# Performance work log

Measured on AMD Instinct MI355X. Metric: run time of the kernel, lower is better.

Reference implementation:

```python
import jax, jax.numpy as jnp
import numpy as np

LEAK = 0.95
THRESHOLD = 1.0
RESCALE = 2.0


def _xavier_uniform(key, shape, gain=2.0):
    fan_out, fan_in = shape
    bound = gain * np.sqrt(6.0 / (fan_in + fan_out))
    return jax.random.uniform(key, shape, jnp.float32, -bound, bound)


def setup_inputs() -> dict:
    key = jax.random.key(0)
    k_inp, k_w1, k_w2 = jax.random.split(key, 3)
    inp = jax.random.normal(k_inp, (8192, 784), jnp.float32)
    w1 = _xavier_uniform(k_w1, (800, 784))   # fc1.weight
    w2 = _xavier_uniform(k_w2, (10, 800))    # fc2.weight
    return {"inp": inp, "w1": w1, "w2": w2, "num_steps": 25}


@jax.custom_vjp
def spike_fn(x):
    return (x > 0).astype(x.dtype)

def _spike_fwd(x):
    return spike_fn(x), x

def _spike_bwd(x, g):
    # grad = g * 0.3 * relu(1 - |x|)  (surrogate BP)
    return (g * 0.3 * jnp.maximum(1.0 - jnp.abs(x), 0.0),)

spike_fn.defvjp(_spike_fwd, _spike_bwd)


def poisson_gen(key, inp):
    r = jax.random.uniform(key, inp.shape, inp.dtype)
    temp = (r * RESCALE <= jnp.abs(inp)).astype(inp.dtype) * jnp.sign(inp)
    return 0.5 * (temp + 1.0)


def reference(inp, w1, w2, num_steps):
    batch = inp.shape[0]
    x = inp.reshape(batch, -1)
    keys = jax.random.split(jax.random.key(42), num_steps)

    def step(carry, key):
        mem1, mem2 = carry
        sp = poisson_gen(key, x)                    # [B, 784]
        mem1 = LEAK * mem1 + (1.0 - LEAK) * (sp @ w1.T)  # [B, 800]
        mem_thr = mem1 / THRESHOLD - 1.0
        out = spike_fn(mem_thr)
        rst = jnp.where(mem_thr > 0, THRESHOLD, 0.0)
        mem1 = mem1 - jax.lax.stop_gradient(rst)
        mem2 = mem2 + out @ w2.T                    # [B, 10]
        return (mem1, mem2), None

    init = (jnp.zeros((batch, 800), x.dtype), jnp.zeros((batch, 10), x.dtype))
    (_, mem2), _ = jax.lax.scan(step, init, keys)
    return mem2 / num_steps
```

## Files before the change

### kernel.cpp

```cpp
#include <hip/hip_runtime.h>
#include <cstdint>

__host__ __device__ inline uint32_t tf_rotl32(uint32_t x, uint32_t r) {
  return (x << r) | (x >> (32u - r));
}

__host__ __device__ inline void threefry2x32(uint32_t k0, uint32_t k1,
                                             uint32_t x0, uint32_t x1,
                                             uint32_t* o0, uint32_t* o1) {
  uint32_t ks0 = k0, ks1 = k1, ks2 = k0 ^ k1 ^ 0x1BD11BDAu;
  x0 += ks0; x1 += ks1;
#define TF_R(r) { x0 += x1; x1 = tf_rotl32(x1, r); x1 ^= x0; }
  TF_R(13) TF_R(15) TF_R(26) TF_R(6)
  x0 += ks1; x1 += ks2 + 1u;
  TF_R(17) TF_R(29) TF_R(16) TF_R(24)
  x0 += ks2; x1 += ks0 + 2u;
  TF_R(13) TF_R(15) TF_R(26) TF_R(6)
  x0 += ks0; x1 += ks1 + 3u;
  TF_R(17) TF_R(29) TF_R(16) TF_R(24)
  x0 += ks1; x1 += ks2 + 4u;
  TF_R(13) TF_R(15) TF_R(26) TF_R(6)
  x0 += ks2; x1 += ks0 + 5u;
#undef TF_R
  *o0 = x0; *o1 = x1;
}

#define BSZ   8192
#define KIN   784
#define HID   800
#define NOUT  10
#define NSTEP 25


__global__ __launch_bounds__(256) void enc_kernel(const float* __restrict__ inp,
                                                  uint8_t* __restrict__ enc,
                                                  uint32_t k0, uint32_t k1) {
  int j = blockIdx.x * blockDim.x + threadIdx.x;
  if (j >= BSZ * KIN) return;
  uint32_t o0, o1;
  threefry2x32(k0, k1, 0u, (uint32_t)j, &o0, &o1);
  uint32_t bits = o0 ^ o1;
  float r = __uint_as_float((bits >> 9) | 0x3f800000u) - 1.0f;
  float x = inp[j];
  bool cond = (2.0f * r <= fabsf(x));
  int s = (x > 0.0f) ? 1 : ((x < 0.0f) ? -1 : 0);
  enc[j] = (uint8_t)(1 + (cond ? s : 0));
}

#define BM 128
#define BN 32
#define BK 8

typedef float f32x2 __attribute__((ext_vector_type(2)));
typedef uint32_t u32;

__device__ __forceinline__ float cvt_ub(u32 x, int i) {
  return (float)((x >> (8 * i)) & 0xffu);
}

__device__ __forceinline__ void gload4(const void* g, void* l) {
  __builtin_amdgcn_global_load_lds(
      (const __attribute__((address_space(1))) void*)g,
      (__attribute__((address_space(3))) void*)l, 4, 0, 0);
}

__device__ __forceinline__ void pk_fma_lo(f32x2& acc, f32x2 a, f32x2 b) {
  asm("v_pk_fma_f32 %0, %1, %2, %0 op_sel:[0,0,0] op_sel_hi:[0,1,1]"
      : "+v"(acc)
      : "v"(a), "v"(b));
}
__device__ __forceinline__ void pk_fma_hi(f32x2& acc, f32x2 a, f32x2 b) {
  asm("v_pk_fma_f32 %0, %1, %2, %0 op_sel:[1,0,0] op_sel_hi:[1,1,1]"
      : "+v"(acc)
      : "v"(a), "v"(b));
}

__global__ __launch_bounds__(256) void gemm_kernel(const uint8_t* __restrict__ enc,
                                                   const float* __restrict__ w1,
                                                   float* __restrict__ gp) {
  __shared__ u32   As[2][BK * BM / 4];
  __shared__ float Bs[2][BK][BN];
  const int panel  = blockIdx.z;
  const int kstart = panel * 264;
  const int ntile  = (panel == 2) ? 32 : 33;
  const int m0 = blockIdx.x * BM;
  const int n0 = blockIdx.y * BN;
  const int t  = threadIdx.x;
  const int lane = t & 63;
  const int wv   = t >> 6;

  const int tm = t / 8;
  const int tn = t % 8;

  const uint8_t* a_src = enc + (size_t)(m0 + (lane >> 1)) * KIN + kstart + (lane & 1) * 4;
  const float*   b_src = w1  + (size_t)(n0 + (lane & 31)) * KIN + kstart + (lane >> 5);

  f32x2 acc[4][2];
#pragma unroll
  for (int mi = 0; mi < 4; mi++)
#pragma unroll
    for (int nj = 0; nj < 2; nj++) acc[mi][nj] = (f32x2)(0.0f);

#define ISSUE(P, TILE)                                                    \
  {                                                                       \
    if (wv == 0) {                                                        \
      _Pragma("unroll")                                                   \
      for (int q = 0; q < 4; q++)                                         \
        gload4(a_src + (size_t)(TILE) * BK + (size_t)(32 * q) * KIN,      \
               &As[P][64 * q]);                                           \
    } else if (wv == 1) {                                                 \
      _Pragma("unroll")                                                   \
      for (int q = 0; q < 4; q++)                                         \
        gload4(b_src + (size_t)(TILE) * BK + 2 * q, &Bs[P][2 * q][0]);    \
    }                                                                     \
  }

  ISSUE(0, 0)
  __syncthreads();

  int p = 0;
  for (int tile = 0; tile < ntile; tile++) {
    if (tile + 1 < ntile) { ISSUE(p ^ 1, tile + 1) }
    const u32* aw = &As[p][tm * 8];
    uint4 qa = *(const uint4*)(aw);
    uint4 qb = *(const uint4*)(aw + 4);
#pragma unroll
    for (int kk = 0; kk < BK; kk++) {
      const u32 w0  = (kk < 4) ? qa.x : qa.y;
      const u32 w1r = (kk < 4) ? qa.z : qa.w;
      const u32 w2  = (kk < 4) ? qb.x : qb.y;
      const u32 w3  = (kk < 4) ? qb.z : qb.w;
      const int sh = kk & 3;
      f32x2 am[2];
      am[0].x = cvt_ub(w0, sh);  am[0].y = cvt_ub(w1r, sh);
      am[1].x = cvt_ub(w2, sh);  am[1].y = cvt_ub(w3, sh);
      float4 bv = *(const float4*)&Bs[p][kk][tn * 4];
      f32x2 b2[2];
      b2[0].x = bv.x; b2[0].y = bv.y;
      b2[1].x = bv.z; b2[1].y = bv.w;
#pragma unroll
      for (int mp = 0; mp < 2; mp++) {
        pk_fma_lo(acc[2 * mp + 0][0], am[mp], b2[0]);
        pk_fma_lo(acc[2 * mp + 0][1], am[mp], b2[1]);
        pk_fma_hi(acc[2 * mp + 1][0], am[mp], b2[0]);
        pk_fma_hi(acc[2 * mp + 1][1], am[mp], b2[1]);
      }
    }
    __syncthreads();
    p ^= 1;
  }
#undef ISSUE

  float* base = gp + (size_t)panel * BSZ * HID;
#pragma unroll
  for (int mi = 0; mi < 4; mi++) {
    float* dst = base + (size_t)(m0 + tm * 4 + mi) * HID + n0 + tn * 4;
    float4 o;
    o.x = acc[mi][0].x;
    o.y = acc[mi][0].y;
    o.z = acc[mi][1].x;
    o.w = acc[mi][1].y;
    *(float4*)dst = o;
  }
}

__global__ __launch_bounds__(256) void update_kernel(const float* __restrict__ gp,
                                                     float* __restrict__ mem1,
                                                     const float* __restrict__ w2,
                                                     float* __restrict__ mem2) {
  __shared__ float w2s[NOUT * HID];
  for (int i = threadIdx.x; i < NOUT * HID; i += 256) w2s[i] = w2[i];
  __syncthreads();

  const int wave = threadIdx.x / 64;
  const int lane = threadIdx.x % 64;
  const int b = blockIdx.x * 4 + wave;

  const size_t GS = (size_t)BSZ * HID;
  const float* g0 = gp + (size_t)b * HID;
  const float* g1 = g0 + GS;
  const float* g2 = g1 + GS;
  float* mrow = mem1 + (size_t)b * HID;

  float acc[NOUT];
#pragma unroll
  for (int i = 0; i < NOUT; i++) acc[i] = 0.0f;

  for (int j = lane; j < HID; j += 64) {
    float gs = __fmul_rn(0.5f, __fadd_rn(__fadd_rn(g0[j], g1[j]), g2[j]));
    float m = __fadd_rn(__fmul_rn(0.95f, mrow[j]), __fmul_rn(0.05f, gs));
    bool spike = __fadd_rn(m, -1.0f) > 0.0f;
    mrow[j] = spike ? __fadd_rn(m, -1.0f) : m;
    if (spike) {
#pragma unroll
      for (int i = 0; i < NOUT; i++) acc[i] += w2s[i * HID + j];
    }
  }
#pragma unroll
  for (int i = 0; i < NOUT; i++) {
    float v = acc[i];
    for (int off = 32; off > 0; off >>= 1) v += __shfl_down(v, off);
    if (lane == 0) mem2[(size_t)b * NOUT + i] += v;
  }
}

__global__ __launch_bounds__(256) void finalize_kernel(const float* __restrict__ mem2,
                                                       const int* __restrict__ ns,
                                                       float* __restrict__ out) {
  int i = blockIdx.x * blockDim.x + threadIdx.x;
  if (i < BSZ * NOUT) out[i] = mem2[i] / (float)(*ns);
}

extern "C" void kernel_launch(void* const* d_in, const int* in_sizes, int n_in,
                              void* d_out, int out_size, void* d_ws, size_t ws_size,
                              hipStream_t stream) {
  const float* inp = (const float*)d_in[0];
  const float* w1  = (const float*)d_in[1];
  const float* w2  = (const float*)d_in[2];
  const int*   dns = (const int*)d_in[3];
  float* out = (float*)d_out;

  char* ws = (char*)d_ws;
  size_t off = 0;
  uint8_t* enc = (uint8_t*)(ws + off);  off += (size_t)BSZ * KIN;
  off = (off + 255) & ~(size_t)255;
  float* gp   = (float*)(ws + off);     off += (size_t)3 * BSZ * HID * 4;
  float* mem1 = (float*)(ws + off);     off += (size_t)BSZ * HID * 4;
  float* mem2 = (float*)(ws + off);     off += (size_t)BSZ * NOUT * 4;

  (void)hipMemsetAsync(mem1, 0, (size_t)BSZ * HID * 4, stream);
  (void)hipMemsetAsync(mem2, 0, (size_t)BSZ * NOUT * 4, stream);

  uint32_t keys[NSTEP][2];
  for (int t = 0; t < NSTEP; t++)
    threefry2x32(0u, 42u, 0u, (uint32_t)t, &keys[t][0], &keys[t][1]);

  const int n_elem = BSZ * KIN;
  for (int t = 0; t < NSTEP; t++) {
    enc_kernel<<<(n_elem + 255) / 256, 256, 0, stream>>>(inp, enc, keys[t][0], keys[t][1]);
    gemm_kernel<<<dim3(BSZ / BM, HID / BN, 3), 256, 0, stream>>>(enc, w1, gp);
    update_kernel<<<BSZ / 4, 256, 0, stream>>>(gp, mem1, w2, mem2);
  }
  finalize_kernel<<<(BSZ * NOUT + 255) / 256, 256, 0, stream>>>(mem2, dns, out);
}
```

Baseline: 4.857 ms.

## Halve GEMM block threads, give each thread 8x4 outputs with padded A tile

The GEMM block drops from 256 to 128 threads, and each thread now computes 8 rows by 4 columns instead of 4 by 4, which doubles register-level reuse of the B fragment. The A shared tile is regrouped with padding (AGRP=68) so each thread reads its 8-row fragment with four 16-byte LDS loads while avoiding bank conflicts. Wave 0 still loads A and wave 1 loads B. Fewer threads per block and more accumulator registers may lower latency hiding and occupancy.

Result: no change. 4.947 ms (+1.9%).

```diff
diff --git a/kernel.cpp b/kernel.cpp
--- a/kernel.cpp
+++ b/kernel.cpp
@@ -50,6 +50,8 @@
 #define BM 128
 #define BN 32
 #define BK 8
+#define AGRP 68
+#define ASZ  (3 * AGRP + 64)
 
 typedef float f32x2 __attribute__((ext_vector_type(2)));
 typedef uint32_t u32;
@@ -75,10 +77,10 @@
       : "v"(a), "v"(b));
 }
 
-__global__ __launch_bounds__(256) void gemm_kernel(const uint8_t* __restrict__ enc,
+__global__ __launch_bounds__(128) void gemm_kernel(const uint8_t* __restrict__ enc,
                                                    const float* __restrict__ w1,
                                                    float* __restrict__ gp) {
-  __shared__ u32   As[2][BK * BM / 4];
+  __shared__ u32   As[2][ASZ];
   __shared__ float Bs[2][BK][BN];
   const int panel  = blockIdx.z;
   const int kstart = panel * 264;
@@ -95,9 +97,9 @@
   const uint8_t* a_src = enc + (size_t)(m0 + (lane >> 1)) * KIN + kstart + (lane & 1) * 4;
   const float*   b_src = w1  + (size_t)(n0 + (lane & 31)) * KIN + kstart + (lane >> 5);
 
-  f32x2 acc[4][2];
-#pragma unroll
-  for (int mi = 0; mi < 4; mi++)
+  f32x2 acc[8][2];
+#pragma unroll
+  for (int mi = 0; mi < 8; mi++)
 #pragma unroll
     for (int nj = 0; nj < 2; nj++) acc[mi][nj] = (f32x2)(0.0f);
 
@@ -107,8 +109,8 @@
       _Pragma("unroll")                                                   \
       for (int q = 0; q < 4; q++)                                         \
         gload4(a_src + (size_t)(TILE) * BK + (size_t)(32 * q) * KIN,      \
-               &As[P][64 * q]);                                           \
-    } else if (wv == 1) {                                                 \
+               &As[P][AGRP * q]);                                         \
+    } else {                                                              \
       _Pragma("unroll")                                                   \
       for (int q = 0; q < 4; q++)                                         \
         gload4(b_src + (size_t)(TILE) * BK + 2 * q, &Bs[P][2 * q][0]);    \
@@ -118,28 +120,38 @@
   ISSUE(0, 0)
   __syncthreads();
 
+  const int afrag = AGRP * (tm >> 2) + 16 * (tm & 3);
+
   int p = 0;
   for (int tile = 0; tile < ntile; tile++) {
     if (tile + 1 < ntile) { ISSUE(p ^ 1, tile + 1) }
-    const u32* aw = &As[p][tm * 8];
-    uint4 qa = *(const uint4*)(aw);
-    uint4 qb = *(const uint4*)(aw + 4);
+    const u32* aw = &As[p][afrag];
+    uint4 q0 = *(const uint4*)(aw);
+    uint4 q1 = *(const uint4*)(aw + 4);
+    uint4 q2 = *(const uint4*)(aw + 8);
+    uint4 q3 = *(const uint4*)(aw + 12);
 #pragma unroll
     for (int kk = 0; kk < BK; kk++) {
-      const u32 w0  = (kk < 4) ? qa.x : qa.y;
-      const u32 w1r = (kk < 4) ? qa.z : qa.w;
-      const u32 w2  = (kk < 4) ? qb.x : qb.y;
-      const u32 w3  = (kk < 4) ? qb.z : qb.w;
       const int sh = kk & 3;
-      f32x2 am[2];
-      am[0].x = cvt_ub(w0, sh);  am[0].y = cvt_ub(w1r, sh);
-      am[1].x = cvt_ub(w2, sh);  am[1].y = cvt_ub(w3, sh);
+      const u32 r0 = (kk < 4) ? q0.x : q0.y;
+      const u32 r1 = (kk < 4) ? q0.z : q0.w;
+      const u32 r2 = (kk < 4) ? q1.x : q1.y;
+      const u32 r3 = (kk < 4) ? q1.z : q1.w;
+      const u32 r4 = (kk < 4) ? q2.x : q2.y;
+      const u32 r5 = (kk < 4) ? q2.z : q2.w;
+      const u32 r6 = (kk < 4) ? q3.x : q3.y;
+      const u32 r7 = (kk < 4) ? q3.z : q3.w;
+      f32x2 am[4];
+      am[0].x = cvt_ub(r0, sh);  am[0].y = cvt_ub(r1, sh);
+      am[1].x = cvt_ub(r2, sh);  am[1].y = cvt_ub(r3, sh);
+      am[2].x = cvt_ub(r4, sh);  am[2].y = cvt_ub(r5, sh);
+      am[3].x = cvt_ub(r6, sh);  am[3].y = cvt_ub(r7, sh);
       float4 bv = *(const float4*)&Bs[p][kk][tn * 4];
       f32x2 b2[2];
       b2[0].x = bv.x; b2[0].y = bv.y;
       b2[1].x = bv.z; b2[1].y = bv.w;
 #pragma unroll
-      for (int mp = 0; mp < 2; mp++) {
+      for (int mp = 0; mp < 4; mp++) {
         pk_fma_lo(acc[2 * mp + 0][0], am[mp], b2[0]);
         pk_fma_lo(acc[2 * mp + 0][1], am[mp], b2[1]);
         pk_fma_hi(acc[2 * mp + 1][0], am[mp], b2[0]);
@@ -153,8 +165,8 @@
 
   float* base = gp + (size_t)panel * BSZ * HID;
 #pragma unroll
-  for (int mi = 0; mi < 4; mi++) {
-    float* dst = base + (size_t)(m0 + tm * 4 + mi) * HID + n0 + tn * 4;
+  for (int mi = 0; mi < 8; mi++) {
+    float* dst = base + (size_t)(m0 + tm * 8 + mi) * HID + n0 + tn * 4;
     float4 o;
     o.x = acc[mi][0].x;
     o.y = acc[mi][0].y;
@@ -238,7 +250,7 @@
   const int n_elem = BSZ * KIN;
   for (int t = 0; t < NSTEP; t++) {
     enc_kernel<<<(n_elem + 255) / 256, 256, 0, stream>>>(inp, enc, keys[t][0], keys[t][1]);
-    gemm_kernel<<<dim3(BSZ / BM, HID / BN, 3), 256, 0, stream>>>(enc, w1, gp);
+    gemm_kernel<<<dim3(BSZ / BM, HID / BN, 3), 128, 0, stream>>>(enc, w1, gp);
     update_kernel<<<BSZ / 4, 256, 0, stream>>>(gp, mem1, w2, mem2);
   }
   finalize_kernel<<<(BSZ * NOUT + 255) / 256, 256, 0, stream>>>(mem2, dns, out);
```

## Restructure hidden GEMM to 512-row tiles with scalar-broadcast transposed weights

Applied to the files above, without the earlier changes.

Adds a one-time transpose of w1 into the workspace so each K-row of weights is contiguous across the output columns. The GEMM is rebuilt around 512x32 block tiles where each thread owns two batch rows and all 32 columns. Weights are read straight from global memory at wave-uniform addresses, which the compiler can turn into scalar loads. Each wave stages only its own spike-encoded A rows in LDS with a BK of 16, so the block-wide barriers are dropped. The trade-offs are plain scalar FMAs instead of packed FMAs, more accumulator registers, fewer blocks in flight, and reliance on correct wait-counts for the async LDS loads.

Result: slower. 5.348 ms (+10.1%).

```diff
diff --git a/kernel.cpp b/kernel.cpp
--- a/kernel.cpp
+++ b/kernel.cpp
@@ -47,11 +47,18 @@
   enc[j] = (uint8_t)(1 + (cond ? s : 0));
 }
 
-#define BM 128
+__global__ __launch_bounds__(256) void transpose_kernel(const float* __restrict__ w1,
+                                                        float* __restrict__ w1t) {
+  int idx = blockIdx.x * blockDim.x + threadIdx.x;
+  if (idx >= KIN * HID) return;
+  int k = idx / HID, n = idx % HID;
+  w1t[idx] = w1[(size_t)n * KIN + k];
+}
+
+#define BM 512
 #define BN 32
-#define BK 8
-
-typedef float f32x2 __attribute__((ext_vector_type(2)));
+#define BK 16
+
 typedef uint32_t u32;
 
 __device__ __forceinline__ float cvt_ub(u32 x, int i) {
@@ -64,103 +71,91 @@
       (__attribute__((address_space(3))) void*)l, 4, 0, 0);
 }
 
-__device__ __forceinline__ void pk_fma_lo(f32x2& acc, f32x2 a, f32x2 b) {
-  asm("v_pk_fma_f32 %0, %1, %2, %0 op_sel:[0,0,0] op_sel_hi:[0,1,1]"
-      : "+v"(acc)
-      : "v"(a), "v"(b));
-}
-__device__ __forceinline__ void pk_fma_hi(f32x2& acc, f32x2 a, f32x2 b) {
-  asm("v_pk_fma_f32 %0, %1, %2, %0 op_sel:[1,0,0] op_sel_hi:[1,1,1]"
-      : "+v"(acc)
-      : "v"(a), "v"(b));
-}
-
 __global__ __launch_bounds__(256) void gemm_kernel(const uint8_t* __restrict__ enc,
-                                                   const float* __restrict__ w1,
+                                                   const float* __restrict__ w1t,
                                                    float* __restrict__ gp) {
-  __shared__ u32   As[2][BK * BM / 4];
-  __shared__ float Bs[2][BK][BN];
+  __shared__ uint8_t As[2][BM * BK];
   const int panel  = blockIdx.z;
   const int kstart = panel * 264;
-  const int ntile  = (panel == 2) ? 32 : 33;
+  const bool htail = (panel != 2);
   const int m0 = blockIdx.x * BM;
   const int n0 = blockIdx.y * BN;
   const int t  = threadIdx.x;
   const int lane = t & 63;
   const int wv   = t >> 6;
 
-  const int tm = t / 8;
-  const int tn = t % 8;
-
-  const uint8_t* a_src = enc + (size_t)(m0 + (lane >> 1)) * KIN + kstart + (lane & 1) * 4;
-  const float*   b_src = w1  + (size_t)(n0 + (lane & 31)) * KIN + kstart + (lane >> 5);
-
-  f32x2 acc[4][2];
-#pragma unroll
-  for (int mi = 0; mi < 4; mi++)
-#pragma unroll
-    for (int nj = 0; nj < 2; nj++) acc[mi][nj] = (f32x2)(0.0f);
+  const uint8_t* a_src = enc + (size_t)(m0 + wv * 128 + (lane >> 2)) * KIN
+                         + kstart + (lane & 3) * 4;
+
+  const int r0 = wv * 128 + lane;
+
+  float acc0[32], acc1[32];
+#pragma unroll
+  for (int c = 0; c < 32; c++) { acc0[c] = 0.0f; acc1[c] = 0.0f; }
 
 #define ISSUE(P, TILE)                                                    \
   {                                                                       \
-    if (wv == 0) {                                                        \
-      _Pragma("unroll")                                                   \
-      for (int q = 0; q < 4; q++)                                         \
-        gload4(a_src + (size_t)(TILE) * BK + (size_t)(32 * q) * KIN,      \
-               &As[P][64 * q]);                                           \
-    } else if (wv == 1) {                                                 \
-      _Pragma("unroll")                                                   \
-      for (int q = 0; q < 4; q++)                                         \
-        gload4(b_src + (size_t)(TILE) * BK + 2 * q, &Bs[P][2 * q][0]);    \
-    }                                                                     \
+    _Pragma("unroll")                                                     \
+    for (int q = 0; q < 8; q++)                                           \
+      gload4(a_src + (size_t)(TILE) * BK + (size_t)(16 * q) * KIN,        \
+             &As[P][wv * 2048 + q * 256]);                                \
   }
 
   ISSUE(0, 0)
-  __syncthreads();
 
   int p = 0;
-  for (int tile = 0; tile < ntile; tile++) {
-    if (tile + 1 < ntile) { ISSUE(p ^ 1, tile + 1) }
-    const u32* aw = &As[p][tm * 8];
-    uint4 qa = *(const uint4*)(aw);
-    uint4 qb = *(const uint4*)(aw + 4);
-#pragma unroll
-    for (int kk = 0; kk < BK; kk++) {
-      const u32 w0  = (kk < 4) ? qa.x : qa.y;
-      const u32 w1r = (kk < 4) ? qa.z : qa.w;
-      const u32 w2  = (kk < 4) ? qb.x : qb.y;
-      const u32 w3  = (kk < 4) ? qb.z : qb.w;
-      const int sh = kk & 3;
-      f32x2 am[2];
-      am[0].x = cvt_ub(w0, sh);  am[0].y = cvt_ub(w1r, sh);
-      am[1].x = cvt_ub(w2, sh);  am[1].y = cvt_ub(w3, sh);
-      float4 bv = *(const float4*)&Bs[p][kk][tn * 4];
-      f32x2 b2[2];
-      b2[0].x = bv.x; b2[0].y = bv.y;
-      b2[1].x = bv.z; b2[1].y = bv.w;
-#pragma unroll
-      for (int mp = 0; mp < 2; mp++) {
-        pk_fma_lo(acc[2 * mp + 0][0], am[mp], b2[0]);
-        pk_fma_lo(acc[2 * mp + 0][1], am[mp], b2[1]);
-        pk_fma_hi(acc[2 * mp + 1][0], am[mp], b2[0]);
-        pk_fma_hi(acc[2 * mp + 1][1], am[mp], b2[1]);
+  for (int tile = 0; tile < 16; tile++) {
+    if (tile < 15) { ISSUE(p ^ 1, tile + 1) }
+    else if (htail) { ISSUE(p ^ 1, 16) }
+    uint4 s0 = *(const uint4*)&As[p][(size_t)r0 * 16];
+    uint4 s1 = *(const uint4*)&As[p][(size_t)(r0 + 64) * 16];
+    const float* tb = w1t + (size_t)(kstart + tile * BK) * HID + n0;
+#pragma unroll
+    for (int kk = 0; kk < 16; kk++) {
+      const u32 wa0[4] = {s0.x, s0.y, s0.z, s0.w};
+      const u32 wa1[4] = {s1.x, s1.y, s1.z, s1.w};
+      float a0 = cvt_ub(wa0[kk >> 2], kk & 3);
+      float a1 = cvt_ub(wa1[kk >> 2], kk & 3);
+      const float* brow = tb + (size_t)kk * HID;
+#pragma unroll
+      for (int c = 0; c < 32; c++) {
+        float b = brow[c];
+        acc0[c] = __builtin_fmaf(a0, b, acc0[c]);
+        acc1[c] = __builtin_fmaf(a1, b, acc1[c]);
       }
     }
-    __syncthreads();
     p ^= 1;
   }
+  if (htail) {
+    uint4 s0 = *(const uint4*)&As[p][(size_t)r0 * 16];
+    uint4 s1 = *(const uint4*)&As[p][(size_t)(r0 + 64) * 16];
+    const float* tb = w1t + (size_t)(kstart + 256) * HID + n0;
+#pragma unroll
+    for (int kk = 0; kk < 8; kk++) {
+      const u32 wa0[2] = {s0.x, s0.y};
+      const u32 wa1[2] = {s1.x, s1.y};
+      float a0 = cvt_ub(wa0[kk >> 2], kk & 3);
+      float a1 = cvt_ub(wa1[kk >> 2], kk & 3);
+      const float* brow = tb + (size_t)kk * HID;
+#pragma unroll
+      for (int c = 0; c < 32; c++) {
+        float b = brow[c];
+        acc0[c] = __builtin_fmaf(a0, b, acc0[c]);
+        acc1[c] = __builtin_fmaf(a1, b, acc1[c]);
+      }
+    }
+  }
 #undef ISSUE
 
-  float* base = gp + (size_t)panel * BSZ * HID;
-#pragma unroll
-  for (int mi = 0; mi < 4; mi++) {
-    float* dst = base + (size_t)(m0 + tm * 4 + mi) * HID + n0 + tn * 4;
-    float4 o;
-    o.x = acc[mi][0].x;
-    o.y = acc[mi][0].y;
-    o.z = acc[mi][1].x;
-    o.w = acc[mi][1].y;
-    *(float4*)dst = o;
+  const size_t GS = (size_t)BSZ * HID;
+  float* o0 = gp + (size_t)panel * GS + (size_t)(m0 + r0) * HID + n0;
+  float* o1 = o0 + (size_t)64 * HID;
+#pragma unroll
+  for (int c = 0; c < 32; c += 4) {
+    float4 v0 = {acc0[c], acc0[c + 1], acc0[c + 2], acc0[c + 3]};
+    float4 v1 = {acc1[c], acc1[c + 1], acc1[c + 2], acc1[c + 3]};
+    *(float4*)(o0 + c) = v0;
+    *(float4*)(o1 + c) = v1;
   }
 }
 
@@ -224,6 +219,7 @@
   size_t off = 0;
   uint8_t* enc = (uint8_t*)(ws + off);  off += (size_t)BSZ * KIN;
   off = (off + 255) & ~(size_t)255;
+  float* w1t  = (float*)(ws + off);     off += (size_t)KIN * HID * 4;
   float* gp   = (float*)(ws + off);     off += (size_t)3 * BSZ * HID * 4;
   float* mem1 = (float*)(ws + off);     off += (size_t)BSZ * HID * 4;
   float* mem2 = (float*)(ws + off);     off += (size_t)BSZ * NOUT * 4;
@@ -231,6 +227,8 @@
   (void)hipMemsetAsync(mem1, 0, (size_t)BSZ * HID * 4, stream);
   (void)hipMemsetAsync(mem2, 0, (size_t)BSZ * NOUT * 4, stream);
 
+  transpose_kernel<<<(KIN * HID + 255) / 256, 256, 0, stream>>>(w1, w1t);
+
   uint32_t keys[NSTEP][2];
   for (int t = 0; t < NSTEP; t++)
     threefry2x32(0u, 42u, 0u, (uint32_t)t, &keys[t][0], &keys[t][1]);
@@ -238,7 +236,7 @@
   const int n_elem = BSZ * KIN;
   for (int t = 0; t < NSTEP; t++) {
     enc_kernel<<<(n_elem + 255) / 256, 256, 0, stream>>>(inp, enc, keys[t][0], keys[t][1]);
-    gemm_kernel<<<dim3(BSZ / BM, HID / BN, 3), 256, 0, stream>>>(enc, w1, gp);
+    gemm_kernel<<<dim3(BSZ / BM, HID / BN, 3), 256, 0, stream>>>(enc, w1t, gp);
     update_kernel<<<BSZ / 4, 256, 0, stream>>>(gp, mem1, w2, mem2);
   }
   finalize_kernel<<<(BSZ * NOUT + 255) / 256, 256, 0, stream>>>(mem2, dns, out);
```
